# Kernel tuning notes

Measured on AMD Instinct MI355X. Metric: run time of the kernel, lower is better.

## Reference

```python
import jax, jax.numpy as jnp
import numpy as np

MARGIN = 1.0  # configs: COSINE_DISTANCE=True, INVERTED_LOSS=True
EPS = 1e-8


def setup_inputs() -> dict:
    key = jax.random.key(0)
    B, d = 8192, 128
    inputs = jax.random.normal(key, (B, d), dtype=jnp.float32)
    return {"inputs": inputs}


def reference(inputs):
    B = inputs.shape[0]
    P = B // 2
    # inverted cosine distance: D = X X^T / 128
    D = jnp.matmul(inputs, inputs.T) / 128.0          # [B, B]
    Dexpm = jnp.exp(MARGIN + D)                       # [B, B]

    # rows pos_i = 2p gather odd columns 2k+1; rows pos_j = 2p+1 gather even columns 2l
    E_io = Dexpm[0::2, 1::2]                          # [P, P]
    E_je = Dexpm[1::2, 0::2]                          # [P, P]

    p = jnp.arange(P)
    k = jnp.arange(P)
    # faithful to original: exclude k == pos_j (=2p+1) and l == pos_i (=2p)
    mask_i = k[None, :] != (2 * p + 1)[:, None]       # [P, P]
    mask_j = k[None, :] != (2 * p)[:, None]           # [P, P]

    neg_ik = jnp.sum(jnp.where(mask_i, E_io, 0.0), axis=1)  # [P]
    neg_jl = jnp.sum(jnp.where(mask_j, E_je, 0.0), axis=1)  # [P]

    D_pos = D[2 * p, 2 * p + 1]                       # [P]
    J = jnp.log(EPS + neg_ik + neg_jl) - D_pos        # inverted loss: log(Dissim) - D_pos
    return jnp.sum(jnp.square(jnp.maximum(J, 0.0))) / B
```

## Files before the change

kernel.cpp:

```cpp
#include <hip/hip_runtime.h>
#include <hip/hip_bf16.h>
#include <math.h>

#define P 4096
#define DIM 128
#define EPS_F 1e-8f
#define LOG2E 1.4426950408889634f
#define LN2   0.6931471805599453f
#define MLG2  LOG2E

#define RPB 128
#define CPB 256
#define TILE_COLS 64
#define NTILES 4
#define NRB (P / RPB)
#define NCB (P / CPB)
#define TILE_STRIDE (TILE_COLS * 2 * DIM)

typedef float f32x4 __attribute__((ext_vector_type(4)));
typedef short bf16x8 __attribute__((ext_vector_type(8)));

static __device__ __forceinline__ short f2bf(float f) {
    return __builtin_bit_cast(short, __float2bfloat16(f));
}

static __device__ __forceinline__ void bload(f32x4* dst, const float* s) {
    #pragma unroll
    for (int u = 0; u < 8; ++u)
        dst[u] = *reinterpret_cast<const f32x4*>(s + u * 4);
}

static __device__ __forceinline__ void cvtwrite(short* lB, const f32x4* regs,
                                                int br, int bko) {
    #pragma unroll
    for (int u = 0; u < 4; ++u) {
        f32x4 lo = regs[2 * u], hi = regs[2 * u + 1];
        bf16x8 v;
        v[0] = f2bf(lo[0]); v[1] = f2bf(lo[1]);
        v[2] = f2bf(lo[2]); v[3] = f2bf(lo[3]);
        v[4] = f2bf(hi[0]); v[5] = f2bf(hi[1]);
        v[6] = f2bf(hi[2]); v[7] = f2bf(hi[3]);
        int idx = (br * DIM + bko + u * 8) ^ ((br & 7) << 3);
        *reinterpret_cast<bf16x8*>(&lB[idx]) = v;
    }
}

__global__ __launch_bounds__(256, 2) void gram_fused(
    const float* __restrict__ x,
    float* __restrict__ pr,
    float* __restrict__ pc,
    float* __restrict__ dv,
    float* __restrict__ civ,
    float* __restrict__ cjv,
    float* __restrict__ out) {

    __shared__ __align__(16) short Bs[2][TILE_COLS * DIM];
    __shared__ float csf[4][CPB];

    const int tid = threadIdx.x;
    const int lane = tid & 63;
    const int wave = tid >> 6;
    const int cb = blockIdx.x;
    const int rb = blockIdx.y;
    const int p0 = rb * RPB;
    const int c0 = cb * CPB;
    const int lrow = lane & 15;
    const int g = lane >> 4;
    const int kgrp = g * 8;

    if (cb == 0 && rb == 0 && tid == 0) out[0] = 0.0f;

    const int br = tid >> 2;
    const int bko = (tid & 3) * 32;
    const float* bbase = x + (size_t)(2 * (c0 + br) + 1) * DIM + bko;

    f32x4 bregA[8], bregB[8];
    bload(bregA, bbase);
    bload(bregB, bbase + TILE_STRIDE);

    bf16x8 a[2][4];
    #pragma unroll
    for (int m = 0; m < 2; ++m) {
        const float* arow =
            x + (size_t)(2 * (p0 + wave * 32 + m * 16 + lrow)) * DIM + kgrp;
        #pragma unroll
        for (int k = 0; k < 4; ++k) {
            f32x4 lo = *reinterpret_cast<const f32x4*>(arow + k * 32);
            f32x4 hi = *reinterpret_cast<const f32x4*>(arow + k * 32 + 4);
            bf16x8 r;
            r[0] = f2bf(lo[0] * (LOG2E / 128.f)); r[1] = f2bf(lo[1] * (LOG2E / 128.f));
            r[2] = f2bf(lo[2] * (LOG2E / 128.f)); r[3] = f2bf(lo[3] * (LOG2E / 128.f));
            r[4] = f2bf(hi[0] * (LOG2E / 128.f)); r[5] = f2bf(hi[1] * (LOG2E / 128.f));
            r[6] = f2bf(hi[2] * (LOG2E / 128.f)); r[7] = f2bf(hi[3] * (LOG2E / 128.f));
            a[m][k] = r;
        }
    }

    cvtwrite(Bs[0], bregA, br, bko);

    float rs[2][4];
    float cpp[NTILES][4];
    #pragma unroll
    for (int m = 0; m < 2; ++m)
        #pragma unroll
        for (int j = 0; j < 4; ++j) rs[m][j] = 0.0f;
    #pragma unroll
    for (int t = 0; t < NTILES; ++t)
        #pragma unroll
        for (int n = 0; n < 4; ++n) cpp[t][n] = 0.0f;

    #pragma unroll
    for (int t = 0; t < NTILES; ++t) {
        __syncthreads();
        if (t + 2 < NTILES)
            bload(((t & 1) == 0) ? bregA : bregB,
                  bbase + (size_t)(t + 2) * TILE_STRIDE);
        if (t + 1 < NTILES)
            cvtwrite(Bs[(t + 1) & 1], ((t & 1) == 0) ? bregB : bregA, br, bko);

        const short* B = Bs[t & 1];
        f32x4 acc[2][4];
        #pragma unroll
        for (int m = 0; m < 2; ++m)
            #pragma unroll
            for (int n = 0; n < 4; ++n)
                acc[m][n] = f32x4{MLG2, MLG2, MLG2, MLG2};

        #pragma unroll
        for (int k32 = 0; k32 < 4; ++k32) {
            #pragma unroll
            for (int n = 0; n < 4; ++n) {
                int cc = n * 16 + lrow;
                int idx = (cc * DIM + k32 * 32 + kgrp) ^ ((cc & 7) << 3);
                bf16x8 b = *reinterpret_cast<const bf16x8*>(&B[idx]);
                #pragma unroll
                for (int m = 0; m < 2; ++m)
                    acc[m][n] = __builtin_amdgcn_mfma_f32_16x16x32_bf16(
                        a[m][k32], b, acc[m][n], 0, 0, 0);
            }
        }

        #pragma unroll
        for (int n = 0; n < 4; ++n) {
            const int C0 = c0 + t * 64 + n * 16;
            const int Cl = C0 + lrow;
            #pragma unroll
            for (int m = 0; m < 2; ++m) {
                const int R0 = p0 + wave * 32 + m * 16;
                const bool pdv = (R0 == C0);
                const bool pci = (C0 + 15 >= 2 * R0 + 1) && (C0 <= 2 * R0 + 31);
                const bool pcj = (R0 + 15 >= 2 * C0) && (R0 <= 2 * C0 + 30);
                #pragma unroll
                for (int j = 0; j < 4; ++j) {
                    float av = acc[m][n][j];
                    float e = exp2f(av);
                    rs[m][j] += e;
                    cpp[t][n] += e;
                    int Rj = R0 + g * 4 + j;
                    if (pdv && Cl == Rj)         dv[Rj] = av;
                    if (pci && Cl == 2 * Rj + 1) civ[Rj] = av;
                    if (pcj && Rj == 2 * Cl)     cjv[Cl] = av;
                }
            }
        }
    }

    #pragma unroll
    for (int m = 0; m < 2; ++m)
        #pragma unroll
        for (int j = 0; j < 4; ++j) {
            float v = rs[m][j];
            v += __shfl_xor(v, 1);
            v += __shfl_xor(v, 2);
            v += __shfl_xor(v, 4);
            v += __shfl_xor(v, 8);
            rs[m][j] = v;
        }
    if (lrow == 0) {
        #pragma unroll
        for (int m = 0; m < 2; ++m)
            #pragma unroll
            for (int j = 0; j < 4; ++j)
                pr[(size_t)cb * P + p0 + wave * 32 + m * 16 + g * 4 + j] =
                    rs[m][j];
    }

    #pragma unroll
    for (int t = 0; t < NTILES; ++t)
        #pragma unroll
        for (int n = 0; n < 4; ++n) {
            float v = cpp[t][n];
            v += __shfl_xor(v, 16);
            v += __shfl_xor(v, 32);
            if (lane < 16)
                csf[wave][t * TILE_COLS + n * 16 + lane] = v;
        }
    __syncthreads();
    if (tid < CPB)
        pc[(size_t)rb * P + c0 + tid] =
            csf[0][tid] + csf[1][tid] + csf[2][tid] + csf[3][tid];
}

__global__ __launch_bounds__(256) void finalize(
    const float* __restrict__ pr,
    const float* __restrict__ pc,
    const float* __restrict__ dv,
    const float* __restrict__ civ,
    const float* __restrict__ cjv,
    float* __restrict__ out) {

    __shared__ float wsum[4];
    const int tid = threadIdx.x;
    const int lane = tid & 63;
    const int wave = tid >> 6;
    const int p = blockIdx.x * 256 + tid;

    float s = 0.0f;
    #pragma unroll
    for (int b = 0; b < NCB; ++b) s += pr[(size_t)b * P + p];
    #pragma unroll
    for (int b = 0; b < NRB; ++b) s += pc[(size_t)b * P + p];

    float corr = 0.0f;
    if (p < P / 2) corr = exp2f(civ[p]) + exp2f(cjv[p]);

    float Dpos = dv[p] * LN2 - 1.0f;
    float J = logf(EPS_F + (s - corr)) - Dpos;
    float r = fmaxf(J, 0.0f);
    r = r * r;

    #pragma unroll
    for (int off = 32; off > 0; off >>= 1) r += __shfl_down(r, off);
    if (lane == 0) wsum[wave] = r;
    __syncthreads();
    if (tid == 0)
        atomicAdd(out, (wsum[0] + wsum[1] + wsum[2] + wsum[3]) *
                           (1.0f / 8192.0f));
}

extern "C" void kernel_launch(void* const* d_in, const int* in_sizes, int n_in,
                              void* d_out, int out_size, void* d_ws, size_t ws_size,
                              hipStream_t stream) {
    const float* x = (const float*)d_in[0];
    float* pr = (float*)d_ws;
    float* pc = pr + (size_t)NCB * P;
    float* dv = pc + (size_t)NRB * P;
    float* civ = dv + P;
    float* cjv = civ + P / 2;

    dim3 grid(NCB, NRB);
    gram_fused<<<grid, 256, 0, stream>>>(x, pr, pc, dv, civ, cjv, (float*)d_out);
    finalize<<<P / 256, 256, 0, stream>>>(pr, pc, dv, civ, cjv, (float*)d_out);
}
```

Measured before the change: 31.27 us.

## Pre-convert and deinterleave inputs to bf16, stage via direct LDS loads, fuse finalize

Adds a pre-pass kernel that converts the fp32 input to bf16, pre-scales the even rows, and splits even and odd rows into separate contiguous buffers. The Gram kernel then streams B tiles straight into shared memory with global_load_lds (swizzle applied to the source address) instead of loading through registers and converting, and it reads A fragments directly as bf16. The separate finalize kernel is replaced by a last-block-done pattern using an atomic counter, where the final block does the reduction serially. This trades one extra kernel launch and a single-block tail reduction for halved operand bandwidth and less register and conversion work in the main loop.

```diff
diff --git a/kernel.cpp b/kernel.cpp
--- a/kernel.cpp
+++ b/kernel.cpp
@@ -15,47 +15,58 @@
 #define NTILES 4
 #define NRB (P / RPB)
 #define NCB (P / CPB)
-#define TILE_STRIDE (TILE_COLS * 2 * DIM)
+#define NBLK (NRB * NCB)
 
 typedef float f32x4 __attribute__((ext_vector_type(4)));
 typedef short bf16x8 __attribute__((ext_vector_type(8)));
 
+static __device__ __forceinline__ void gload_lds16(const void* g, void* l) {
+    __builtin_amdgcn_global_load_lds(
+        (const __attribute__((address_space(1))) void*)g,
+        (__attribute__((address_space(3))) void*)l,
+        16, 0, 0);
+}
+
 static __device__ __forceinline__ short f2bf(float f) {
     return __builtin_bit_cast(short, __float2bfloat16(f));
 }
 
-static __device__ __forceinline__ void bload(f32x4* dst, const float* s) {
-    #pragma unroll
-    for (int u = 0; u < 8; ++u)
-        dst[u] = *reinterpret_cast<const f32x4*>(s + u * 4);
-}
-
-static __device__ __forceinline__ void cvtwrite(short* lB, const f32x4* regs,
-                                                int br, int bko) {
-    #pragma unroll
-    for (int u = 0; u < 4; ++u) {
-        f32x4 lo = regs[2 * u], hi = regs[2 * u + 1];
-        bf16x8 v;
-        v[0] = f2bf(lo[0]); v[1] = f2bf(lo[1]);
-        v[2] = f2bf(lo[2]); v[3] = f2bf(lo[3]);
-        v[4] = f2bf(hi[0]); v[5] = f2bf(hi[1]);
-        v[6] = f2bf(hi[2]); v[7] = f2bf(hi[3]);
-        int idx = (br * DIM + bko + u * 8) ^ ((br & 7) << 3);
-        *reinterpret_cast<bf16x8*>(&lB[idx]) = v;
-    }
-}
-
-__global__ __launch_bounds__(256, 2) void gram_fused(
+__global__ __launch_bounds__(256) void convert_deint(
     const float* __restrict__ x,
+    short* __restrict__ xe,
+    short* __restrict__ xo,
+    unsigned int* __restrict__ cnt) {
+
+    const int idx = blockIdx.x * 256 + threadIdx.x;
+    const int row = idx >> 5;
+    const int c4 = idx & 31;
+
+    f32x4 v = *reinterpret_cast<const f32x4*>(x + (size_t)idx * 4);
+    const bool odd = row & 1;
+    const float s = odd ? 1.0f : (LOG2E / 128.0f);
+    short4 pk;
+    pk.x = f2bf(v[0] * s); pk.y = f2bf(v[1] * s);
+    pk.z = f2bf(v[2] * s); pk.w = f2bf(v[3] * s);
+    short* dst = odd ? xo : xe;
+    *reinterpret_cast<short4*>(&dst[(size_t)(row >> 1) * DIM + c4 * 4]) = pk;
+
+    if (idx == 0) *cnt = 0;
+}
+
+__global__ __launch_bounds__(256, 2) void gram_last(
+    const short* __restrict__ xe,
+    const short* __restrict__ xo,
     float* __restrict__ pr,
     float* __restrict__ pc,
     float* __restrict__ dv,
     float* __restrict__ civ,
     float* __restrict__ cjv,
+    unsigned int* __restrict__ cnt,
     float* __restrict__ out) {
 
     __shared__ __align__(16) short Bs[2][TILE_COLS * DIM];
     __shared__ float csf[4][CPB];
+    __shared__ unsigned int sOld;
 
     const int tid = threadIdx.x;
     const int lane = tid & 63;
@@ -68,35 +79,29 @@
     const int g = lane >> 4;
     const int kgrp = g * 8;
 
-    if (cb == 0 && rb == 0 && tid == 0) out[0] = 0.0f;
-
-    const int br = tid >> 2;
-    const int bko = (tid & 3) * 32;
-    const float* bbase = x + (size_t)(2 * (c0 + br) + 1) * DIM + bko;
-
-    f32x4 bregA[8], bregB[8];
-    bload(bregA, bbase);
-    bload(bregB, bbase + TILE_STRIDE);
+    const char* gB = (const char*)(xo + (size_t)c0 * DIM);
+    auto stage = [&](int t) {
+        char* lB = (char*)Bs[t & 1];
+        const char* gt = gB + (size_t)t * (TILE_COLS * DIM * 2);
+        #pragma unroll
+        for (int i = 0; i < 4; ++i) {
+            int Lbase = (wave * 4 + i) * 1024;
+            int L = Lbase + lane * 16;
+            int src = L ^ (((L >> 8) & 7) << 4);
+            gload_lds16(gt + src, lB + Lbase);
+        }
+    };
+    stage(0);
 
     bf16x8 a[2][4];
     #pragma unroll
     for (int m = 0; m < 2; ++m) {
-        const float* arow =
-            x + (size_t)(2 * (p0 + wave * 32 + m * 16 + lrow)) * DIM + kgrp;
-        #pragma unroll
-        for (int k = 0; k < 4; ++k) {
-            f32x4 lo = *reinterpret_cast<const f32x4*>(arow + k * 32);
-            f32x4 hi = *reinterpret_cast<const f32x4*>(arow + k * 32 + 4);
-            bf16x8 r;
-            r[0] = f2bf(lo[0] * (LOG2E / 128.f)); r[1] = f2bf(lo[1] * (LOG2E / 128.f));
-            r[2] = f2bf(lo[2] * (LOG2E / 128.f)); r[3] = f2bf(lo[3] * (LOG2E / 128.f));
-            r[4] = f2bf(hi[0] * (LOG2E / 128.f)); r[5] = f2bf(hi[1] * (LOG2E / 128.f));
-            r[6] = f2bf(hi[2] * (LOG2E / 128.f)); r[7] = f2bf(hi[3] * (LOG2E / 128.f));
-            a[m][k] = r;
-        }
-    }
-
-    cvtwrite(Bs[0], bregA, br, bko);
+        const short* arow =
+            xe + (size_t)(p0 + wave * 32 + m * 16 + lrow) * DIM + kgrp;
+        #pragma unroll
+        for (int k32 = 0; k32 < 4; ++k32)
+            a[m][k32] = *reinterpret_cast<const bf16x8*>(arow + k32 * 32);
+    }
 
     float rs[2][4];
     float cpp[NTILES][4];
@@ -112,11 +117,7 @@
     #pragma unroll
     for (int t = 0; t < NTILES; ++t) {
         __syncthreads();
-        if (t + 2 < NTILES)
-            bload(((t & 1) == 0) ? bregA : bregB,
-                  bbase + (size_t)(t + 2) * TILE_STRIDE);
-        if (t + 1 < NTILES)
-            cvtwrite(Bs[(t + 1) & 1], ((t & 1) == 0) ? bregB : bregA, br, bko);
+        if (t + 1 < NTILES) stage(t + 1);
 
         const short* B = Bs[t & 1];
         f32x4 acc[2][4];
@@ -199,43 +200,46 @@
     if (tid < CPB)
         pc[(size_t)rb * P + c0 + tid] =
             csf[0][tid] + csf[1][tid] + csf[2][tid] + csf[3][tid];
-}
-
-__global__ __launch_bounds__(256) void finalize(
-    const float* __restrict__ pr,
-    const float* __restrict__ pc,
-    const float* __restrict__ dv,
-    const float* __restrict__ civ,
-    const float* __restrict__ cjv,
-    float* __restrict__ out) {
-
-    __shared__ float wsum[4];
-    const int tid = threadIdx.x;
-    const int lane = tid & 63;
-    const int wave = tid >> 6;
-    const int p = blockIdx.x * 256 + tid;
-
-    float s = 0.0f;
-    #pragma unroll
-    for (int b = 0; b < NCB; ++b) s += pr[(size_t)b * P + p];
-    #pragma unroll
-    for (int b = 0; b < NRB; ++b) s += pc[(size_t)b * P + p];
-
-    float corr = 0.0f;
-    if (p < P / 2) corr = exp2f(civ[p]) + exp2f(cjv[p]);
-
-    float Dpos = dv[p] * LN2 - 1.0f;
-    float J = logf(EPS_F + (s - corr)) - Dpos;
-    float r = fmaxf(J, 0.0f);
-    r = r * r;
-
-    #pragma unroll
-    for (int off = 32; off > 0; off >>= 1) r += __shfl_down(r, off);
-    if (lane == 0) wsum[wave] = r;
-    __syncthreads();
-    if (tid == 0)
-        atomicAdd(out, (wsum[0] + wsum[1] + wsum[2] + wsum[3]) *
-                           (1.0f / 8192.0f));
+
+    __syncthreads();
+    if (tid == 0) {
+        __threadfence();
+        sOld = __hip_atomic_fetch_add(cnt, 1u, __ATOMIC_ACQ_REL,
+                                      __HIP_MEMORY_SCOPE_AGENT);
+    }
+    __syncthreads();
+    if (sOld != NBLK - 1) return;
+
+    __threadfence();
+
+    float racc = 0.0f;
+    #pragma unroll
+    for (int q = 0; q < P / 256; ++q) {
+        const int p = q * 256 + tid;
+        float s = 0.0f;
+        #pragma unroll
+        for (int b = 0; b < NCB; ++b) s += pr[(size_t)b * P + p];
+        #pragma unroll
+        for (int b = 0; b < NRB; ++b) s += pc[(size_t)b * P + p];
+
+        float corr = 0.0f;
+        if (p < P / 2) corr = exp2f(civ[p]) + exp2f(cjv[p]);
+
+        float Dpos = dv[p] * LN2 - 1.0f;
+        float J = logf(EPS_F + (s - corr)) - Dpos;
+        float r = fmaxf(J, 0.0f);
+        racc += r * r;
+    }
+
+    #pragma unroll
+    for (int off = 32; off > 0; off >>= 1) racc += __shfl_down(racc, off);
+    if (lane == 0) csf[0][wave] = racc;
+    __syncthreads();
+    if (tid == 0) {
+        out[0] = (csf[0][0] + csf[0][1] + csf[0][2] + csf[0][3]) *
+                 (1.0f / 8192.0f);
+        *cnt = 0;
+    }
 }
 
 extern "C" void kernel_launch(void* const* d_in, const int* in_sizes, int n_in,
@@ -247,8 +251,12 @@
     float* dv = pc + (size_t)NRB * P;
     float* civ = dv + P;
     float* cjv = civ + P / 2;
-
+    short* xe = (short*)(cjv + P / 2);
+    short* xo = xe + (size_t)P * DIM;
+    unsigned int* cnt = (unsigned int*)(xo + (size_t)P * DIM);
+
+    convert_deint<<<1024, 256, 0, stream>>>(x, xe, xo, cnt);
     dim3 grid(NCB, NRB);
-    gram_fused<<<grid, 256, 0, stream>>>(x, pr, pc, dv, civ, cjv, (float*)d_out);
-    finalize<<<P / 256, 256, 0, stream>>>(pr, pc, dv, civ, cjv, (float*)d_out);
-}
+    gram_last<<<grid, 256, 0, stream>>>(xe, xo, pr, pc, dv, civ, cjv, cnt,
+                                        (float*)d_out);
+}
```

After: 107.4 us. +243.4%, slower.

## Pre-convert inputs to bf16 MFMA-fragment layout and drop LDS staging

Applied to the files above, without the earlier changes.

Adds a pre-pass kernel that converts the fp32 input to bf16, applies the log2e/128 scale to even rows, and de-interleaves even and odd rows into a tiled layout matching MFMA fragment order. The gram kernel then loads A and B fragments directly from global memory, with no LDS double-buffering, register conversion or block barriers. The aim is to stop every block from redundantly converting the same B columns. The cost is an extra kernel launch plus a workspace round trip, and B fragments now come from global/L2 rather than shared memory.

```diff
diff --git a/kernel.cpp b/kernel.cpp
--- a/kernel.cpp
+++ b/kernel.cpp
@@ -11,11 +11,9 @@
 
 #define RPB 128
 #define CPB 256
-#define TILE_COLS 64
 #define NTILES 4
 #define NRB (P / RPB)
 #define NCB (P / CPB)
-#define TILE_STRIDE (TILE_COLS * 2 * DIM)
 
 typedef float f32x4 __attribute__((ext_vector_type(4)));
 typedef short bf16x8 __attribute__((ext_vector_type(8)));
@@ -24,29 +22,34 @@
     return __builtin_bit_cast(short, __float2bfloat16(f));
 }
 
-static __device__ __forceinline__ void bload(f32x4* dst, const float* s) {
-    #pragma unroll
-    for (int u = 0; u < 8; ++u)
-        dst[u] = *reinterpret_cast<const f32x4*>(s + u * 4);
-}
-
-static __device__ __forceinline__ void cvtwrite(short* lB, const f32x4* regs,
-                                                int br, int bko) {
-    #pragma unroll
-    for (int u = 0; u < 4; ++u) {
-        f32x4 lo = regs[2 * u], hi = regs[2 * u + 1];
-        bf16x8 v;
-        v[0] = f2bf(lo[0]); v[1] = f2bf(lo[1]);
-        v[2] = f2bf(lo[2]); v[3] = f2bf(lo[3]);
-        v[4] = f2bf(hi[0]); v[5] = f2bf(hi[1]);
-        v[6] = f2bf(hi[2]); v[7] = f2bf(hi[3]);
-        int idx = (br * DIM + bko + u * 8) ^ ((br & 7) << 3);
-        *reinterpret_cast<bf16x8*>(&lB[idx]) = v;
-    }
-}
-
-__global__ __launch_bounds__(256, 2) void gram_fused(
+#define TILE16(t16, k32) (((t16) * 4 + (k32)) * 512)
+
+__global__ __launch_bounds__(256) void convert_deint(
     const float* __restrict__ x,
+    short* __restrict__ xeT,
+    short* __restrict__ xoT) {
+
+    const int idx = blockIdx.x * 256 + threadIdx.x;
+    const int row = idx >> 5;
+    const int k0 = (idx & 31) * 4;
+
+    f32x4 v = *reinterpret_cast<const f32x4*>(x + (size_t)idx * 4);
+    const bool odd = row & 1;
+    const float s = odd ? 1.0f : (LOG2E / 128.0f);
+    short4 pk;
+    pk.x = f2bf(v[0] * s); pk.y = f2bf(v[1] * s);
+    pk.z = f2bf(v[2] * s); pk.w = f2bf(v[3] * s);
+
+    const int C = row >> 1;
+    const int di = TILE16(C >> 4, k0 >> 5) +
+                   ((C & 15) * 4 + ((k0 >> 3) & 3)) * 8 + (k0 & 7);
+    short* dst = odd ? xoT : xeT;
+    *reinterpret_cast<short4*>(&dst[di]) = pk;
+}
+
+__global__ __launch_bounds__(256, 2) void gram_mfma(
+    const short* __restrict__ xeT,
+    const short* __restrict__ xoT,
     float* __restrict__ pr,
     float* __restrict__ pc,
     float* __restrict__ dv,
@@ -54,7 +57,6 @@
     float* __restrict__ cjv,
     float* __restrict__ out) {
 
-    __shared__ __align__(16) short Bs[2][TILE_COLS * DIM];
     __shared__ float csf[4][CPB];
 
     const int tid = threadIdx.x;
@@ -66,37 +68,18 @@
     const int c0 = cb * CPB;
     const int lrow = lane & 15;
     const int g = lane >> 4;
-    const int kgrp = g * 8;
+    const int loff = (lrow * 4 + g) * 8;
 
     if (cb == 0 && rb == 0 && tid == 0) out[0] = 0.0f;
 
-    const int br = tid >> 2;
-    const int bko = (tid & 3) * 32;
-    const float* bbase = x + (size_t)(2 * (c0 + br) + 1) * DIM + bko;
-
-    f32x4 bregA[8], bregB[8];
-    bload(bregA, bbase);
-    bload(bregB, bbase + TILE_STRIDE);
-
+    const int at16 = (p0 >> 4) + wave * 2;
     bf16x8 a[2][4];
     #pragma unroll
-    for (int m = 0; m < 2; ++m) {
-        const float* arow =
-            x + (size_t)(2 * (p0 + wave * 32 + m * 16 + lrow)) * DIM + kgrp;
-        #pragma unroll
-        for (int k = 0; k < 4; ++k) {
-            f32x4 lo = *reinterpret_cast<const f32x4*>(arow + k * 32);
-            f32x4 hi = *reinterpret_cast<const f32x4*>(arow + k * 32 + 4);
-            bf16x8 r;
-            r[0] = f2bf(lo[0] * (LOG2E / 128.f)); r[1] = f2bf(lo[1] * (LOG2E / 128.f));
-            r[2] = f2bf(lo[2] * (LOG2E / 128.f)); r[3] = f2bf(lo[3] * (LOG2E / 128.f));
-            r[4] = f2bf(hi[0] * (LOG2E / 128.f)); r[5] = f2bf(hi[1] * (LOG2E / 128.f));
-            r[6] = f2bf(hi[2] * (LOG2E / 128.f)); r[7] = f2bf(hi[3] * (LOG2E / 128.f));
-            a[m][k] = r;
-        }
-    }
-
-    cvtwrite(Bs[0], bregA, br, bko);
+    for (int m = 0; m < 2; ++m)
+        #pragma unroll
+        for (int k32 = 0; k32 < 4; ++k32)
+            a[m][k32] = *reinterpret_cast<const bf16x8*>(
+                &xeT[TILE16(at16 + m, k32) + loff]);
 
     float rs[2][4];
     float cpp[NTILES][4];
@@ -109,16 +92,10 @@
         #pragma unroll
         for (int n = 0; n < 4; ++n) cpp[t][n] = 0.0f;
 
+    const int bt16 = c0 >> 4;
+
     #pragma unroll
     for (int t = 0; t < NTILES; ++t) {
-        __syncthreads();
-        if (t + 2 < NTILES)
-            bload(((t & 1) == 0) ? bregA : bregB,
-                  bbase + (size_t)(t + 2) * TILE_STRIDE);
-        if (t + 1 < NTILES)
-            cvtwrite(Bs[(t + 1) & 1], ((t & 1) == 0) ? bregB : bregA, br, bko);
-
-        const short* B = Bs[t & 1];
         f32x4 acc[2][4];
         #pragma unroll
         for (int m = 0; m < 2; ++m)
@@ -128,16 +105,17 @@
 
         #pragma unroll
         for (int k32 = 0; k32 < 4; ++k32) {
-            #pragma unroll
-            for (int n = 0; n < 4; ++n) {
-                int cc = n * 16 + lrow;
-                int idx = (cc * DIM + k32 * 32 + kgrp) ^ ((cc & 7) << 3);
-                bf16x8 b = *reinterpret_cast<const bf16x8*>(&B[idx]);
+            bf16x8 b[4];
+            #pragma unroll
+            for (int n = 0; n < 4; ++n)
+                b[n] = *reinterpret_cast<const bf16x8*>(
+                    &xoT[TILE16(bt16 + t * 4 + n, k32) + loff]);
+            #pragma unroll
+            for (int n = 0; n < 4; ++n)
                 #pragma unroll
                 for (int m = 0; m < 2; ++m)
                     acc[m][n] = __builtin_amdgcn_mfma_f32_16x16x32_bf16(
-                        a[m][k32], b, acc[m][n], 0, 0, 0);
-            }
+                        a[m][k32], b[n], acc[m][n], 0, 0, 0);
         }
 
         #pragma unroll
@@ -193,7 +171,7 @@
             v += __shfl_xor(v, 16);
             v += __shfl_xor(v, 32);
             if (lane < 16)
-                csf[wave][t * TILE_COLS + n * 16 + lane] = v;
+                csf[wave][t * 64 + n * 16 + lane] = v;
         }
     __syncthreads();
     if (tid < CPB)
@@ -247,8 +225,12 @@
     float* dv = pc + (size_t)NRB * P;
     float* civ = dv + P;
     float* cjv = civ + P / 2;
-
+    short* xeT = (short*)(cjv + P / 2);
+    short* xoT = xeT + (size_t)P * DIM;
+
+    convert_deint<<<1024, 256, 0, stream>>>(x, xeT, xoT);
     dim3 grid(NCB, NRB);
-    gram_fused<<<grid, 256, 0, stream>>>(x, pr, pc, dv, civ, cjv, (float*)d_out);
+    gram_mfma<<<grid, 256, 0, stream>>>(xeT, xoT, pr, pc, dv, civ, cjv,
+                                        (float*)d_out);
     finalize<<<P / 256, 256, 0, stream>>>(pr, pc, dv, civ, cjv, (float*)d_out);
 }
```

Result: slower. 35.80 us (+14.5%).
